# Kernel optimization log

Hardware: AMD Instinct MI355X
Metric: run time of the kernel (lower is better)

## Reference

```python
import jax, jax.numpy as jnp
import numpy as np

N = 20000
E = 320000
IN_DIM, HID, OUT_DIM = 32, 64, 4
HEADS = 4
NEG_SLOPE = 0.2


def _self_loops(src, dst):
    loop = jnp.arange(N, dtype=src.dtype)
    return jnp.concatenate([src, loop]), jnp.concatenate([dst, loop])


def gcn_conv(x, W, b, src, dst):
    h = x @ W                                            # [N, C]
    es, ed = _self_loops(src, dst)
    deg = jax.ops.segment_sum(jnp.ones_like(es, dtype=h.dtype), ed, num_segments=N)
    dinv = jnp.where(deg > 0, jax.lax.rsqrt(deg), 0.0)
    norm = dinv[es] * dinv[ed]                           # [E']
    out = jax.ops.segment_sum(h[es] * norm[:, None], ed, num_segments=N)
    return out + b


def gat_conv(x, W, att_src, att_dst, b, src, dst):
    # PyG GATConv: heads concat, self-loops, leaky_relu(0.2), softmax over incoming edges per dst
    H, C = att_src.shape
    h = (x @ W).reshape(N, H, C)                         # [N, H, C]
    a_s = jnp.sum(h * att_src, axis=-1)                  # [N, H]
    a_d = jnp.sum(h * att_dst, axis=-1)                  # [N, H]
    es, ed = _self_loops(src, dst)
    logits = jax.nn.leaky_relu(a_s[es] + a_d[ed], NEG_SLOPE)   # [E', H]
    m = jax.ops.segment_max(logits, ed, num_segments=N)
    expv = jnp.exp(logits - m[ed])
    denom = jax.ops.segment_sum(expv, ed, num_segments=N)
    alpha = expv / denom[ed]                             # [E', H]
    out = jax.ops.segment_sum(h[es] * alpha[:, :, None], ed, num_segments=N)
    return out.reshape(N, H * C) + b


def setup_inputs() -> dict:
    key = jax.random.key(0)
    ks = iter(jax.random.split(key, 32))
    s = 0.05
    def w(shape):
        return jax.random.normal(next(ks), shape, dtype=jnp.float32) * s
    inp = {}
    inp["x"] = jax.random.normal(next(ks), (N, IN_DIM), dtype=jnp.float32)
    inp["edge_index"] = jax.random.randint(next(ks), (2, E), 0, N, dtype=jnp.int32)
    # encoder1 GCN 32->64; encoder2 GCN 64->128; encoder3 GAT 128->128 x4 heads
    inp["w_e1"], inp["b_e1"] = w((IN_DIM, HID)), jnp.zeros((HID,), jnp.float32)
    inp["w_e2"], inp["b_e2"] = w((HID, 2 * HID)), jnp.zeros((2 * HID,), jnp.float32)
    inp["w_e3"] = w((2 * HID, HEADS * 2 * HID))
    inp["as_e3"], inp["ad_e3"] = w((HEADS, 2 * HID)), w((HEADS, 2 * HID))
    inp["b_e3"] = jnp.zeros((HEADS * 2 * HID,), jnp.float32)
    # decoder1 GCN 1024->128; decoder2 GCN 128->64; decoder3 GAT 64->64 x4 heads
    inp["w_d1"], inp["b_d1"] = w((HEADS * 2 * HID, 2 * HID)), jnp.zeros((2 * HID,), jnp.float32)
    inp["w_d2"], inp["b_d2"] = w((2 * HID, HID)), jnp.zeros((HID,), jnp.float32)
    inp["w_d3"] = w((HID, HEADS * HID))
    inp["as_d3"], inp["ad_d3"] = w((HEADS, HID)), w((HEADS, HID))
    inp["b_d3"] = jnp.zeros((HEADS * HID,), jnp.float32)
    # MLP head 256->256->128->4
    inp["w_fc1"], inp["b_fc1"] = w((4 * HID, 4 * HID)), jnp.zeros((4 * HID,), jnp.float32)
    inp["w_fc2"], inp["b_fc2"] = w((4 * HID, 2 * HID)), jnp.zeros((2 * HID,), jnp.float32)
    inp["w_fin"], inp["b_fin"] = w((2 * HID, OUT_DIM)), jnp.zeros((OUT_DIM,), jnp.float32)
    return inp


def reference(x, edge_index, w_e1, b_e1, w_e2, b_e2, w_e3, as_e3, ad_e3, b_e3,
              w_d1, b_d1, w_d2, b_d2, w_d3, as_d3, ad_d3, b_d3,
              w_fc1, b_fc1, w_fc2, b_fc2, w_fin, b_fin):
    src, dst = edge_index[0], edge_index[1]
    relu = jax.nn.relu
    x1 = relu(gcn_conv(x, w_e1, b_e1, src, dst))
    x2 = relu(gcn_conv(x1, w_e2, b_e2, src, dst))
    x3 = relu(gat_conv(x2, w_e3, as_e3, ad_e3, b_e3, src, dst))
    h = relu(gcn_conv(x3, w_d1, b_d1, src, dst)) + x2
    h = relu(gcn_conv(h, w_d2, b_d2, src, dst)) + x1
    h = relu(gat_conv(h, w_d3, as_d3, ad_d3, b_d3, src, dst))
    h = relu(h @ w_fc1 + b_fc1)
    h = relu(h @ w_fc2 + b_fc2)
    return h @ w_fin + b_fin
```

## Files before the change

### kernel.cpp

```cpp
#include <hip/hip_runtime.h>
#include <cstdint>
#include <cstddef>

static constexpr int Nn = 20000;
static constexpr int Ee = 320000;

typedef _Float16 half8 __attribute__((ext_vector_type(8)));
typedef float f32x4 __attribute__((ext_vector_type(4)));

__device__ __forceinline__ float lrelu02(float x){ return fmaxf(x, 0.2f*x); }

__device__ __forceinline__ void packhl(float v, unsigned short& h, unsigned short& l){
  _Float16 hh = (_Float16)v;
  _Float16 ll = (_Float16)((v - (float)hh) * 2048.0f);
  h = __builtin_bit_cast(unsigned short, hh);
  l = __builtin_bit_cast(unsigned short, ll);
}

__global__ void k_count(const int* __restrict__ dst, int* __restrict__ cnt){
  int e = blockIdx.x*256 + threadIdx.x;
  if (e < Ee) atomicAdd(&cnt[dst[e]], 1);
}

__global__ void k_scan(const int* __restrict__ cnt, int* __restrict__ row_start,
                       float* __restrict__ dinv){
  __shared__ int part[1024];
  int tid = threadIdx.x;
  const int PER = 20;
  int base = tid*PER;
  int s = 0;
  for (int i = 0; i < PER; ++i){ int idx = base+i; if (idx < Nn) s += cnt[idx]; }
  part[tid] = s; __syncthreads();
  for (int off = 1; off < 1024; off <<= 1){
    int v = (tid >= off) ? part[tid-off] : 0;
    __syncthreads();
    part[tid] += v;
    __syncthreads();
  }
  int run = (tid == 0) ? 0 : part[tid-1];
  for (int i = 0; i < PER; ++i){
    int idx = base+i;
    if (idx < Nn){
      row_start[idx] = run;
      int c = cnt[idx];
      run += c;
      dinv[idx] = rsqrtf((float)(c+1));
    }
  }
  if (tid == 1023) row_start[Nn] = run;
}

__global__ void k_scatter(const int* __restrict__ src, const int* __restrict__ dst,
                          const int* __restrict__ row_start, int* __restrict__ fill,
                          int* __restrict__ csr){
  int e = blockIdx.x*256 + threadIdx.x;
  if (e < Ee){
    int d = dst[e];
    int pos = row_start[d] + atomicAdd(&fill[d], 1);
    csr[pos] = src[e];
  }
}

__global__ void k_packw(const float* __restrict__ W, unsigned short* __restrict__ out, int n){
  int i = blockIdx.x*256 + threadIdx.x;
  if (i < n){
    unsigned short h,l; packhl(W[i],h,l);
    out[i] = h; out[i+n] = l;
  }
}

template<int C, int POST>
__global__ __launch_bounds__(256) void k_gcn_agg(
    const float* __restrict__ h, const float* __restrict__ dinv,
    const int* __restrict__ row_start, const int* __restrict__ csr,
    const float* __restrict__ bias, const float* __restrict__ skip,
    float* __restrict__ outf, unsigned short* __restrict__ outp){
  int v = blockIdx.x*4 + (threadIdx.x >> 6);
  int lane = threadIdx.x & 63;
  int s = row_start[v], e = row_start[v+1];
  float dv = dinv[v];
  const int c = (C==32) ? (lane & 31) : ((C==128) ? lane*2 : lane);

  float a0 = 0.f, a1 = 0.f;
  for (int base = s; base < e; base += 64){
    int i = base + lane;
    int u = 0; float du = 0.f;
    if (i < e){ u = csr[i]; du = dinv[u]; }
    int cnt = min(64, e - base);
    int j = 0;
    for (; j + 4 <= cnt; j += 4){
      int u0=__shfl(u,j), u1=__shfl(u,j+1), u2=__shfl(u,j+2), u3=__shfl(u,j+3);
      float d0=__shfl(du,j), d1=__shfl(du,j+1), d2=__shfl(du,j+2), d3=__shfl(du,j+3);
      if constexpr (C == 128){
        float2 t0 = *(const float2*)&h[(size_t)u0*128 + c];
        float2 t1 = *(const float2*)&h[(size_t)u1*128 + c];
        float2 t2 = *(const float2*)&h[(size_t)u2*128 + c];
        float2 t3 = *(const float2*)&h[(size_t)u3*128 + c];
        a0=fmaf(d0,t0.x,a0); a1=fmaf(d0,t0.y,a1);
        a0=fmaf(d1,t1.x,a0); a1=fmaf(d1,t1.y,a1);
        a0=fmaf(d2,t2.x,a0); a1=fmaf(d2,t2.y,a1);
        a0=fmaf(d3,t3.x,a0); a1=fmaf(d3,t3.y,a1);
      } else {
        float t0 = h[(size_t)u0*C + c];
        float t1 = h[(size_t)u1*C + c];
        float t2 = h[(size_t)u2*C + c];
        float t3 = h[(size_t)u3*C + c];
        a0=fmaf(d0,t0,a0); a0=fmaf(d1,t1,a0); a0=fmaf(d2,t2,a0); a0=fmaf(d3,t3,a0);
      }
    }
    for (; j < cnt; ++j){
      int uj = __shfl(u,j); float dj = __shfl(du,j);
      if constexpr (C == 128){
        float2 t = *(const float2*)&h[(size_t)uj*128 + c];
        a0 = fmaf(dj, t.x, a0); a1 = fmaf(dj, t.y, a1);
      } else {
        a0 = fmaf(dj, h[(size_t)uj*C + c], a0);
      }
    }
  }

  if constexpr (C == 128){
    float2 hv = *(const float2*)&h[(size_t)v*128 + c];
    float vx = fmaf(a0, dv, hv.x*dv*dv);
    float vy = fmaf(a1, dv, hv.y*dv*dv);
    if constexpr (POST & 1){
      float2 bv = *(const float2*)&bias[c];
      float2 sk = *(const float2*)&skip[(size_t)v*128 + c];
      vx = fmaxf(vx + bv.x, 0.f) + sk.x;
      vy = fmaxf(vy + bv.y, 0.f) + sk.y;
    }
    if constexpr (POST & 2){
      unsigned short h0,l0,h1,l1; packhl(vx,h0,l0); packhl(vy,h1,l1);
      *(unsigned int*)&outp[(size_t)v*128 + c] = (unsigned)h0 | ((unsigned)h1<<16);
      *(unsigned int*)&outp[(size_t)v*128 + c + (size_t)Nn*128] = (unsigned)l0 | ((unsigned)l1<<16);
    } else {
      *(float2*)&outf[(size_t)v*128 + c] = make_float2(vx, vy);
    }
  } else if constexpr (C == 64){
    float val = fmaf(a0, dv, h[(size_t)v*64 + c]*dv*dv);
    if constexpr (POST & 1){
      val = fmaxf(val + bias[c], 0.f) + skip[(size_t)v*64 + c];
    }
    if constexpr (POST & 2){
      unsigned short hh,ll; packhl(val,hh,ll);
      outp[(size_t)v*64 + c] = hh;
      outp[(size_t)v*64 + c + (size_t)Nn*64] = ll;
    } else {
      outf[(size_t)v*64 + c] = val;
    }
  } else {
    float val = fmaf(a0, dv, h[(size_t)v*32 + c]*dv*dv);
    if (lane < 32){
      unsigned short hh,ll; packhl(val,hh,ll);
      outp[(size_t)v*32 + c] = hh;
      outp[(size_t)v*32 + c + (size_t)Nn*32] = ll;
    }
  }
}

template<int INC, int C>
__global__ void k_fold(const float* __restrict__ W, const float* __restrict__ as_,
                       const float* __restrict__ ad_, float* __restrict__ wsF,
                       float* __restrict__ wdF){
  int h = threadIdx.x >> 6, lane = threadIdx.x & 63;
  for (int k = lane; k < INC; k += 64){
    float s = 0.f, d = 0.f;
    #pragma unroll 4
    for (int c = 0; c < C; ++c){
      float wv = W[(size_t)k*(4*C) + h*C + c];
      s = fmaf(wv, as_[h*C + c], s);
      d = fmaf(wv, ad_[h*C + c], d);
    }
    wsF[h*INC + k] = s;
    wdF[h*INC + k] = d;
  }
}

template<int INC>
__global__ __launch_bounds__(256) void k_attn_in(
    const float* __restrict__ X, const float* __restrict__ wsF, const float* __restrict__ wdF,
    float* __restrict__ aS, float* __restrict__ aD){
  int v = blockIdx.x*4 + (threadIdx.x >> 6);
  int lane = threadIdx.x & 63;
  float x0 = X[(size_t)v*INC + lane];
  float x1 = (INC == 128) ? X[(size_t)v*INC + 64 + lane] : 0.f;
  float s[4], d[4];
  #pragma unroll
  for (int h = 0; h < 4; ++h){
    s[h] = x0*wsF[h*INC + lane];
    d[h] = x0*wdF[h*INC + lane];
    if constexpr (INC == 128){
      s[h] = fmaf(x1, wsF[h*INC + 64 + lane], s[h]);
      d[h] = fmaf(x1, wdF[h*INC + 64 + lane], d[h]);
    }
  }
  #pragma unroll
  for (int off = 32; off; off >>= 1){
    #pragma unroll
    for (int h = 0; h < 4; ++h){
      s[h] += __shfl_xor(s[h], off);
      d[h] += __shfl_xor(d[h], off);
    }
  }
  if (lane == 0){
    *(float4*)&aS[v*4] = make_float4(s[0], s[1], s[2], s[3]);
    *(float4*)&aD[v*4] = make_float4(d[0], d[1], d[2], d[3]);
  }
}

template<int INC>
__global__ __launch_bounds__(256) void k_gat_agg_in(
    const float* __restrict__ X, const float* __restrict__ aS, const float* __restrict__ aD,
    const int* __restrict__ row_start, const int* __restrict__ csr,
    unsigned short* __restrict__ outp){
  int v = blockIdx.x*4 + (threadIdx.x >> 6);
  int lane = threadIdx.x & 63;
  int s0 = row_start[v], e0 = row_start[v+1];

  float4 tD = *(const float4*)&aD[v*4];
  float ad0=tD.x, ad1=tD.y, ad2=tD.z, ad3=tD.w;
  float4 tS = *(const float4*)&aS[v*4];
  float ls0=lrelu02(tS.x+ad0), ls1=lrelu02(tS.y+ad1), ls2=lrelu02(tS.z+ad2), ls3=lrelu02(tS.w+ad3);

  float m0=ls0, m1=ls1, m2=ls2, m3=ls3;
  for (int i = s0 + lane; i < e0; i += 64){
    int u = csr[i];
    float4 a4 = *(const float4*)&aS[u*4];
    m0 = fmaxf(m0, lrelu02(a4.x+ad0));
    m1 = fmaxf(m1, lrelu02(a4.y+ad1));
    m2 = fmaxf(m2, lrelu02(a4.z+ad2));
    m3 = fmaxf(m3, lrelu02(a4.w+ad3));
  }
  #pragma unroll
  for (int off = 32; off; off >>= 1){
    m0 = fmaxf(m0, __shfl_xor(m0, off));
    m1 = fmaxf(m1, __shfl_xor(m1, off));
    m2 = fmaxf(m2, __shfl_xor(m2, off));
    m3 = fmaxf(m3, __shfl_xor(m3, off));
  }

  float sd0=0.f, sd1=0.f, sd2=0.f, sd3=0.f;
  float2 acc0={0,0}, acc1={0,0}, acc2={0,0}, acc3={0,0};
  float ac0=0.f, ac1=0.f, ac2=0.f, ac3=0.f;
  const int c2 = lane*2;

  for (int base = s0; base < e0; base += 64){
    int i = base + lane;
    int u = 0; float e0v=0.f, e1v=0.f, e2v=0.f, e3v=0.f;
    if (i < e0){
      u = csr[i];
      float4 a4 = *(const float4*)&aS[u*4];
      e0v = __expf(lrelu02(a4.x+ad0) - m0);
      e1v = __expf(lrelu02(a4.y+ad1) - m1);
      e2v = __expf(lrelu02(a4.z+ad2) - m2);
      e3v = __expf(lrelu02(a4.w+ad3) - m3);
      sd0 += e0v; sd1 += e1v; sd2 += e2v; sd3 += e3v;
    }
    int cnt = min(64, e0 - base);
    #pragma unroll 2
    for (int j = 0; j < cnt; ++j){
      int uj = __shfl(u, j);
      float f0=__shfl(e0v,j), f1=__shfl(e1v,j), f2=__shfl(e2v,j), f3=__shfl(e3v,j);
      if constexpr (INC == 128){
        float2 xu = *(const float2*)&X[(size_t)uj*128 + c2];
        acc0.x=fmaf(f0,xu.x,acc0.x); acc0.y=fmaf(f0,xu.y,acc0.y);
        acc1.x=fmaf(f1,xu.x,acc1.x); acc1.y=fmaf(f1,xu.y,acc1.y);
        acc2.x=fmaf(f2,xu.x,acc2.x); acc2.y=fmaf(f2,xu.y,acc2.y);
        acc3.x=fmaf(f3,xu.x,acc3.x); acc3.y=fmaf(f3,xu.y,acc3.y);
      } else {
        float xu = X[(size_t)uj*64 + lane];
        ac0=fmaf(f0,xu,ac0); ac1=fmaf(f1,xu,ac1); ac2=fmaf(f2,xu,ac2); ac3=fmaf(f3,xu,ac3);
      }
    }
  }

  #pragma unroll
  for (int off = 32; off; off >>= 1){
    sd0 += __shfl_xor(sd0, off);
    sd1 += __shfl_xor(sd1, off);
    sd2 += __shfl_xor(sd2, off);
    sd3 += __shfl_xor(sd3, off);
  }
  float es0=__expf(ls0-m0), es1=__expf(ls1-m1), es2=__expf(ls2-m2), es3=__expf(ls3-m3);
  float r0=1.f/(sd0+es0), r1=1.f/(sd1+es1), r2=1.f/(sd2+es2), r3=1.f/(sd3+es3);

  if constexpr (INC == 128){
    float2 xv = *(const float2*)&X[(size_t)v*128 + c2];
    const size_t loOff = (size_t)Nn*512;
    float ox, oy; unsigned short h0,l0,h1,l1;
    ox=(acc0.x+es0*xv.x)*r0; oy=(acc0.y+es0*xv.y)*r0;
    packhl(ox,h0,l0); packhl(oy,h1,l1);
    *(unsigned int*)&outp[(size_t)v*512 +   0 + c2] = (unsigned)h0|((unsigned)h1<<16);
    *(unsigned int*)&outp[(size_t)v*512 +   0 + c2 + loOff] = (unsigned)l0|((unsigned)l1<<16);
    ox=(acc1.x+es1*xv.x)*r1; oy=(acc1.y+es1*xv.y)*r1;
    packhl(ox,h0,l0); packhl(oy,h1,l1);
    *(unsigned int*)&outp[(size_t)v*512 + 128 + c2] = (unsigned)h0|((unsigned)h1<<16);
    *(unsigned int*)&outp[(size_t)v*512 + 128 + c2 + loOff] = (unsigned)l0|((unsigned)l1<<16);
    ox=(acc2.x+es2*xv.x)*r2; oy=(acc2.y+es2*xv.y)*r2;
    packhl(ox,h0,l0); packhl(oy,h1,l1);
    *(unsigned int*)&outp[(size_t)v*512 + 256 + c2] = (unsigned)h0|((unsigned)h1<<16);
    *(unsigned int*)&outp[(size_t)v*512 + 256 + c2 + loOff] = (unsigned)l0|((unsigned)l1<<16);
    ox=(acc3.x+es3*xv.x)*r3; oy=(acc3.y+es3*xv.y)*r3;
    packhl(ox,h0,l0); packhl(oy,h1,l1);
    *(unsigned int*)&outp[(size_t)v*512 + 384 + c2] = (unsigned)h0|((unsigned)h1<<16);
    *(unsigned int*)&outp[(size_t)v*512 + 384 + c2 + loOff] = (unsigned)l0|((unsigned)l1<<16);
  } else {
    float xv = X[(size_t)v*64 + lane];
    const size_t loOff = (size_t)Nn*256;
    unsigned short hh,ll;
    float o;
    o = (ac0+es0*xv)*r0; packhl(o,hh,ll);
    outp[(size_t)v*256 +   0 + lane] = hh; outp[(size_t)v*256 +   0 + lane + loOff] = ll;
    o = (ac1+es1*xv)*r1; packhl(o,hh,ll);
    outp[(size_t)v*256 +  64 + lane] = hh; outp[(size_t)v*256 +  64 + lane + loOff] = ll;
    o = (ac2+es2*xv)*r2; packhl(o,hh,ll);
    outp[(size_t)v*256 + 128 + lane] = hh; outp[(size_t)v*256 + 128 + lane + loOff] = ll;
    o = (ac3+es3*xv)*r3; packhl(o,hh,ll);
    outp[(size_t)v*256 + 192 + lane] = hh; outp[(size_t)v*256 + 192 + lane + loOff] = ll;
  }
}

template<int K, int J, int Jh, int EPI>
__global__ __launch_bounds__(256) void k_gemm(
    const unsigned short* __restrict__ Ahi, int lda,
    const unsigned short* __restrict__ Whi,
    const float* __restrict__ bias,
    float* __restrict__ outf, unsigned short* __restrict__ outp){
  __shared__ unsigned short sAhi[2*64*8], sAlo[2*64*8];
  __shared__ unsigned short sBhi[4*64*8], sBlo[4*64*8];

  const int tid  = threadIdx.x;
  const int lane = tid & 63, w = tid >> 6;
  const int rh = w & 1, ch = w >> 1;
  const int rb = blockIdx.x;
  const int colbase = blockIdx.z*Jh + blockIdx.y*64;
  const int akoff   = blockIdx.z*K;
  const size_t AloOff = (size_t)Nn*lda;
  const size_t WloOff = (size_t)K*J;

  f32x4 accH0 = {0,0,0,0}, accH1 = {0,0,0,0};
  f32x4 accM0 = {0,0,0,0}, accM1 = {0,0,0,0};

  const int arow = tid >> 3;
  const int ak4  = (tid & 7) * 4;
  const int aw_idx = (((arow>>4)*4 + (ak4>>3))*16 + (arow&15))*8 + (ak4&4);
  const unsigned short* Ag = Ahi + (size_t)(rb*32 + arow)*lda + akoff + ak4;
  const int bcol = tid & 63;
  const int bkg  = tid >> 6;
  const int bw_idx = (((bcol>>4)*4 + bkg)*16 + (bcol&15))*8;
  const unsigned short* Wg = Whi + colbase + bcol;

  #pragma unroll 1
  for (int ks = 0; ks < K/32; ++ks){
    if (ks) __syncthreads();
    {
      const unsigned short* p = Ag + ks*32;
      uint2 hv = *(const uint2*)p;
      uint2 lv = *(const uint2*)(p + AloOff);
      *(uint2*)&sAhi[aw_idx] = hv;
      *(uint2*)&sAlo[aw_idx] = lv;
    }
    {
      const unsigned short* p = Wg + (size_t)(ks*32 + bkg*8)*J;
      unsigned short h[8], l[8];
      #pragma unroll
      for (int i = 0; i < 8; ++i){
        h[i] = p[(size_t)i*J];
        l[i] = p[(size_t)i*J + WloOff];
      }
      uint4 hv, lv;
      hv.x = (unsigned)h[0]|((unsigned)h[1]<<16); hv.y = (unsigned)h[2]|((unsigned)h[3]<<16);
      hv.z = (unsigned)h[4]|((unsigned)h[5]<<16); hv.w = (unsigned)h[6]|((unsigned)h[7]<<16);
      lv.x = (unsigned)l[0]|((unsigned)l[1]<<16); lv.y = (unsigned)l[2]|((unsigned)l[3]<<16);
      lv.z = (unsigned)l[4]|((unsigned)l[5]<<16); lv.w = (unsigned)l[6]|((unsigned)l[7]<<16);
      *(uint4*)&sBhi[bw_idx] = hv;
      *(uint4*)&sBlo[bw_idx] = lv;
    }
    __syncthreads();

    half8 aH = *(const half8*)&sAhi[(rh*64 + lane)*8];
    half8 aL = *(const half8*)&sAlo[(rh*64 + lane)*8];
    {
      int cf = ch*2;
      half8 bH = *(const half8*)&sBhi[(cf*64 + lane)*8];
      half8 bL = *(const half8*)&sBlo[(cf*64 + lane)*8];
      accH0 = __builtin_amdgcn_mfma_f32_16x16x32_f16(aH, bH, accH0, 0, 0, 0);
      accM0 = __builtin_amdgcn_mfma_f32_16x16x32_f16(aH, bL, accM0, 0, 0, 0);
      accM0 = __builtin_amdgcn_mfma_f32_16x16x32_f16(aL, bH, accM0, 0, 0, 0);
    }
    {
      int cf = ch*2 + 1;
      half8 bH = *(const half8*)&sBhi[(cf*64 + lane)*8];
      half8 bL = *(const half8*)&sBlo[(cf*64 + lane)*8];
      accH1 = __builtin_amdgcn_mfma_f32_16x16x32_f16(aH, bH, accH1, 0, 0, 0);
      accM1 = __builtin_amdgcn_mfma_f32_16x16x32_f16(aH, bL, accM1, 0, 0, 0);
      accM1 = __builtin_amdgcn_mfma_f32_16x16x32_f16(aL, bH, accM1, 0, 0, 0);
    }
  }

  #pragma unroll
  for (int q = 0; q < 2; ++q){
    int cf = ch*2 + q;
    int col = colbase + cf*16 + (lane & 15);
    float bv = (EPI >= 1) ? bias[col] : 0.f;
    const f32x4& aH = q ? accH1 : accH0;
    const f32x4& aM = q ? accM1 : accM0;
    #pragma unroll
    for (int r = 0; r < 4; ++r){
      int row = rb*32 + rh*16 + ((lane>>4)*4 + r);
      float v = aH[r] + aM[r]*(1.0f/2048.0f);
      if constexpr (EPI >= 1) v = fmaxf(v + bv, 0.f);
      if constexpr (EPI == 2){
        unsigned short hh, ll; packhl(v, hh, ll);
        outp[(size_t)row*J + col] = hh;
        outp[(size_t)row*J + col + (size_t)Nn*J] = ll;
      } else {
        outf[(size_t)row*J + col] = v;
      }
    }
  }
}

__global__ __launch_bounds__(256) void k_mm_fin(
    const float* __restrict__ A, const float* __restrict__ W,
    const float* __restrict__ bias, float* __restrict__ out){
  int row = blockIdx.x*4 + (threadIdx.x >> 6);
  int lane = threadIdx.x & 63;
  float a0 = A[(size_t)row*128 + lane];
  float a1 = A[(size_t)row*128 + 64 + lane];
  float4 w0 = ((const float4*)W)[lane];
  float4 w1 = ((const float4*)W)[64 + lane];
  float p0 = fmaf(a1, w1.x, a0*w0.x);
  float p1 = fmaf(a1, w1.y, a0*w0.y);
  float p2 = fmaf(a1, w1.z, a0*w0.z);
  float p3 = fmaf(a1, w1.w, a0*w0.w);
  #pragma unroll
  for (int off = 32; off; off >>= 1){
    p0 += __shfl_xor(p0, off);
    p1 += __shfl_xor(p1, off);
    p2 += __shfl_xor(p2, off);
    p3 += __shfl_xor(p3, off);
  }
  if (lane == 0){
    float4 bv = *(const float4*)bias;
    *(float4*)&out[(size_t)row*4] = make_float4(p0+bv.x, p1+bv.y, p2+bv.z, p3+bv.w);
  }
}

extern "C" void kernel_launch(void* const* d_in, const int* in_sizes, int n_in,
                              void* d_out, int out_size, void* d_ws, size_t ws_size,
                              hipStream_t stream){
  const float* x     = (const float*)d_in[0];
  const int*   ei    = (const int*)  d_in[1];
  const float* w_e1  = (const float*)d_in[2];
  const float* b_e1  = (const float*)d_in[3];
  const float* w_e2  = (const float*)d_in[4];
  const float* b_e2  = (const float*)d_in[5];
  const float* w_e3  = (const float*)d_in[6];
  const float* as_e3 = (const float*)d_in[7];
  const float* ad_e3 = (const float*)d_in[8];
  const float* b_e3  = (const float*)d_in[9];
  const float* w_d1  = (const float*)d_in[10];
  const float* b_d1  = (const float*)d_in[11];
  const float* w_d2  = (const float*)d_in[12];
  const float* b_d2  = (const float*)d_in[13];
  const float* w_d3  = (const float*)d_in[14];
  const float* as_d3 = (const float*)d_in[15];
  const float* ad_d3 = (const float*)d_in[16];
  const float* b_d3  = (const float*)d_in[17];
  const float* w_fc1 = (const float*)d_in[18];
  const float* b_fc1 = (const float*)d_in[19];
  const float* w_fc2 = (const float*)d_in[20];
  const float* b_fc2 = (const float*)d_in[21];
  const float* w_fin = (const float*)d_in[22];
  const float* b_fin = (const float*)d_in[23];

  char* ws = (char*)d_ws;
  size_t off = 0;
  auto alloc = [&](size_t bytes)->char*{
    char* p = ws + off;
    off += (bytes + 127) & ~size_t(127);
    return p;
  };
  int*   cnt       = (int*)  alloc((size_t)Nn*4);
  int*   fill      = (int*)  alloc((size_t)Nn*4);
  int*   row_start = (int*)  alloc((size_t)(Nn+1)*4);
  int*   csr       = (int*)  alloc((size_t)Ee*4);
  float* dinv      = (float*)alloc((size_t)Nn*4);
  float* aSb       = (float*)alloc((size_t)Nn*16);
  float* aDb       = (float*)alloc((size_t)Nn*16);
  float* wsF_e3    = (float*)alloc(4*128*4);
  float* wdF_e3    = (float*)alloc(4*128*4);
  float* wsF_d3    = (float*)alloc(4*64*4);
  float* wdF_d3    = (float*)alloc(4*64*4);
  unsigned short* wp_e1  = (unsigned short*)alloc((size_t)32*64*4);
  unsigned short* wp_e2  = (unsigned short*)alloc((size_t)64*128*4);
  unsigned short* wp_e3  = (unsigned short*)alloc((size_t)128*512*4);
  unsigned short* wp_d1  = (unsigned short*)alloc((size_t)512*128*4);
  unsigned short* wp_d2  = (unsigned short*)alloc((size_t)128*64*4);
  unsigned short* wp_d3  = (unsigned short*)alloc((size_t)64*256*4);
  unsigned short* wp_fc1 = (unsigned short*)alloc((size_t)256*256*4);
  unsigned short* wp_fc2 = (unsigned short*)alloc((size_t)256*128*4);
  unsigned short* P0 = (unsigned short*)alloc((size_t)Nn*32*4);
  float* X1 = (float*)alloc((size_t)Nn*64*4);
  float* X2 = (float*)alloc((size_t)Nn*128*4);
  unsigned short* S1 = (unsigned short*)alloc((size_t)Nn*512*4);
  unsigned short* S2 = (unsigned short*)alloc((size_t)Nn*512*4);
  char*  S3 = alloc((size_t)Nn*128*4);

  const int* srcp = ei;
  const int* dstp = ei + Ee;

  hipMemsetAsync(cnt, 0, (size_t)Nn*4, stream);
  hipMemsetAsync(fill, 0, (size_t)Nn*4, stream);
  k_count<<<(Ee+255)/256, 256, 0, stream>>>(dstp, cnt);
  k_scan<<<1, 1024, 0, stream>>>(cnt, row_start, dinv);
  k_scatter<<<(Ee+255)/256, 256, 0, stream>>>(srcp, dstp, row_start, fill, csr);
  k_fold<128,128><<<1, 256, 0, stream>>>(w_e3, as_e3, ad_e3, wsF_e3, wdF_e3);
  k_fold<64,64><<<1, 256, 0, stream>>>(w_d3, as_d3, ad_d3, wsF_d3, wdF_d3);
  k_packw<<<  8, 256, 0, stream>>>(w_e1,  wp_e1,  32*64);
  k_packw<<< 32, 256, 0, stream>>>(w_e2,  wp_e2,  64*128);
  k_packw<<<256, 256, 0, stream>>>(w_e3,  wp_e3,  128*512);
  k_packw<<<256, 256, 0, stream>>>(w_d1,  wp_d1,  512*128);
  k_packw<<< 32, 256, 0, stream>>>(w_d2,  wp_d2,  128*64);
  k_packw<<< 64, 256, 0, stream>>>(w_d3,  wp_d3,  64*256);
  k_packw<<<256, 256, 0, stream>>>(w_fc1, wp_fc1, 256*256);
  k_packw<<<128, 256, 0, stream>>>(w_fc2, wp_fc2, 256*128);

  k_gcn_agg<32,2><<<Nn/4, 256, 0, stream>>>(x, dinv, row_start, csr, nullptr, nullptr, nullptr, P0);
  k_gemm<32,64,64,1><<<dim3(625,1,1), 256, 0, stream>>>(P0, 32, wp_e1, b_e1, X1, nullptr);
  k_gcn_agg<64,2><<<Nn/4, 256, 0, stream>>>(X1, dinv, row_start, csr, nullptr, nullptr, nullptr, (unsigned short*)S3);
  k_gemm<64,128,128,1><<<dim3(625,2,1), 256, 0, stream>>>((unsigned short*)S3, 64, wp_e2, b_e2, X2, nullptr);
  k_attn_in<128><<<Nn/4, 256, 0, stream>>>(X2, wsF_e3, wdF_e3, aSb, aDb);
  k_gat_agg_in<128><<<Nn/4, 256, 0, stream>>>(X2, aSb, aDb, row_start, csr, S1);
  k_gemm<128,512,128,2><<<dim3(625,2,4), 256, 0, stream>>>(S1, 512, wp_e3, b_e3, nullptr, S2);
  k_gemm<512,128,128,0><<<dim3(625,2,1), 256, 0, stream>>>(S2, 512, wp_d1, nullptr, (float*)S3, nullptr);
  k_gcn_agg<128,3><<<Nn/4, 256, 0, stream>>>((float*)S3, dinv, row_start, csr, b_d1, X2, nullptr, S1);
  k_gemm<128,64,64,0><<<dim3(625,1,1), 256, 0, stream>>>(S1, 128, wp_d2, nullptr, (float*)S2, nullptr);
  k_gcn_agg<64,1><<<Nn/4, 256, 0, stream>>>((float*)S2, dinv, row_start, csr, b_d2, X1, (float*)S3, nullptr);
  k_attn_in<64><<<Nn/4, 256, 0, stream>>>((float*)S3, wsF_d3, wdF_d3, aSb, aDb);
  k_gat_agg_in<64><<<Nn/4, 256, 0, stream>>>((float*)S3, aSb, aDb, row_start, csr, S1);
  k_gemm<64,256,64,2><<<dim3(625,1,4), 256, 0, stream>>>(S1, 256, wp_d3, b_d3, nullptr, S2);
  k_gemm<256,256,256,2><<<dim3(625,4,1), 256, 0, stream>>>(S2, 256, wp_fc1, b_fc1, nullptr, S1);
  k_gemm<256,128,128,1><<<dim3(625,2,1), 256, 0, stream>>>(S1, 256, wp_fc2, b_fc2, (float*)S2, nullptr);
  k_mm_fin<<<Nn/4, 256, 0, stream>>>((float*)S2, w_fin, b_fin, (float*)d_out);
}
```

Baseline: 401.5 us.

## Precompute edge records, split GAT softmax prep, pre-tile GEMM weights

Builds an interleaved (src, dinv[src]) edge record array once, so GCN aggregation reads one record per edge with wave-uniform loads instead of shuffles and a dependent dinv gather. The C=32 case now splits the edges between the two half-waves. GAT aggregation is split into a prep kernel that writes per-edge exp weights and per-node normalisers, followed by a scan-free aggregation kernel. Weights are packed directly into the GEMM's shared-memory tile layout, so B tiles load as 16-byte vectors instead of strided scalar loads. The cost is extra global traffic for the alpha and edge-record arrays and two more kernel launches.

```diff
diff --git a/kernel.cpp b/kernel.cpp
--- a/kernel.cpp
+++ b/kernel.cpp
@@ -9,6 +9,7 @@
 typedef float f32x4 __attribute__((ext_vector_type(4)));
 
 __device__ __forceinline__ float lrelu02(float x){ return fmaxf(x, 0.2f*x); }
+__device__ __forceinline__ float af(int x){ return __int_as_float(x); }
 
 __device__ __forceinline__ void packhl(float v, unsigned short& h, unsigned short& l){
   _Float16 hh = (_Float16)v;
@@ -61,61 +62,88 @@
   }
 }
 
-__global__ void k_packw(const float* __restrict__ W, unsigned short* __restrict__ out, int n){
+__global__ void k_erec(const int* __restrict__ csr, const float* __restrict__ dinv,
+                       int2* __restrict__ erec){
   int i = blockIdx.x*256 + threadIdx.x;
-  if (i < n){
-    unsigned short h,l; packhl(W[i],h,l);
-    out[i] = h; out[i+n] = l;
+  if (i < Ee){
+    int u = csr[i];
+    erec[i] = make_int2(u, __float_as_int(dinv[u]));
+  }
+}
+
+template<int K, int J>
+__global__ void k_packwf(const float* __restrict__ W, unsigned short* __restrict__ out){
+  int i = blockIdx.x*256 + threadIdx.x;
+  if (i < K*J){
+    int k = i / J, col = i - k*J;
+    unsigned short h, l; packhl(W[i], h, l);
+    size_t pos = ((size_t)((col>>4)*(K/8) + (k>>3))*16 + (col&15))*8 + (k&7);
+    out[pos] = h;
+    out[pos + (size_t)K*J] = l;
   }
 }
 
 template<int C, int POST>
 __global__ __launch_bounds__(256) void k_gcn_agg(
     const float* __restrict__ h, const float* __restrict__ dinv,
-    const int* __restrict__ row_start, const int* __restrict__ csr,
+    const int* __restrict__ row_start, const int2* __restrict__ erec,
     const float* __restrict__ bias, const float* __restrict__ skip,
     float* __restrict__ outf, unsigned short* __restrict__ outp){
   int v = blockIdx.x*4 + (threadIdx.x >> 6);
   int lane = threadIdx.x & 63;
-  int s = row_start[v], e = row_start[v+1];
+  int s = __builtin_amdgcn_readfirstlane(row_start[v]);
+  int e = __builtin_amdgcn_readfirstlane(row_start[v+1]);
   float dv = dinv[v];
   const int c = (C==32) ? (lane & 31) : ((C==128) ? lane*2 : lane);
 
   float a0 = 0.f, a1 = 0.f;
-  for (int base = s; base < e; base += 64){
-    int i = base + lane;
-    int u = 0; float du = 0.f;
-    if (i < e){ u = csr[i]; du = dinv[u]; }
-    int cnt = min(64, e - base);
-    int j = 0;
-    for (; j + 4 <= cnt; j += 4){
-      int u0=__shfl(u,j), u1=__shfl(u,j+1), u2=__shfl(u,j+2), u3=__shfl(u,j+3);
-      float d0=__shfl(du,j), d1=__shfl(du,j+1), d2=__shfl(du,j+2), d3=__shfl(du,j+3);
-      if constexpr (C == 128){
-        float2 t0 = *(const float2*)&h[(size_t)u0*128 + c];
-        float2 t1 = *(const float2*)&h[(size_t)u1*128 + c];
-        float2 t2 = *(const float2*)&h[(size_t)u2*128 + c];
-        float2 t3 = *(const float2*)&h[(size_t)u3*128 + c];
-        a0=fmaf(d0,t0.x,a0); a1=fmaf(d0,t0.y,a1);
-        a0=fmaf(d1,t1.x,a0); a1=fmaf(d1,t1.y,a1);
-        a0=fmaf(d2,t2.x,a0); a1=fmaf(d2,t2.y,a1);
-        a0=fmaf(d3,t3.x,a0); a1=fmaf(d3,t3.y,a1);
-      } else {
-        float t0 = h[(size_t)u0*C + c];
-        float t1 = h[(size_t)u1*C + c];
-        float t2 = h[(size_t)u2*C + c];
-        float t3 = h[(size_t)u3*C + c];
-        a0=fmaf(d0,t0,a0); a0=fmaf(d1,t1,a0); a0=fmaf(d2,t2,a0); a0=fmaf(d3,t3,a0);
-      }
-    }
-    for (; j < cnt; ++j){
-      int uj = __shfl(u,j); float dj = __shfl(du,j);
-      if constexpr (C == 128){
-        float2 t = *(const float2*)&h[(size_t)uj*128 + c];
-        a0 = fmaf(dj, t.x, a0); a1 = fmaf(dj, t.y, a1);
-      } else {
-        a0 = fmaf(dj, h[(size_t)uj*C + c], a0);
-      }
+  if constexpr (C == 32){
+    int half = lane >> 5;
+    int j = s + half;
+    for (; j + 2 < e; j += 4){
+      int2 r0 = erec[j], r1 = erec[j+2];
+      float t0 = h[(size_t)r0.x*32 + c];
+      float t1 = h[(size_t)r1.x*32 + c];
+      a0 = fmaf(af(r0.y), t0, a0);
+      a0 = fmaf(af(r1.y), t1, a0);
+    }
+    if (j < e){
+      int2 r0 = erec[j];
+      a0 = fmaf(af(r0.y), h[(size_t)r0.x*32 + c], a0);
+    }
+    a0 += __shfl_xor(a0, 32);
+  } else if constexpr (C == 128){
+    int j = s;
+    for (; j + 4 <= e; j += 4){
+      int2 r0 = erec[j], r1 = erec[j+1], r2 = erec[j+2], r3 = erec[j+3];
+      float2 t0 = *(const float2*)&h[(size_t)r0.x*128 + c];
+      float2 t1 = *(const float2*)&h[(size_t)r1.x*128 + c];
+      float2 t2 = *(const float2*)&h[(size_t)r2.x*128 + c];
+      float2 t3 = *(const float2*)&h[(size_t)r3.x*128 + c];
+      a0=fmaf(af(r0.y),t0.x,a0); a1=fmaf(af(r0.y),t0.y,a1);
+      a0=fmaf(af(r1.y),t1.x,a0); a1=fmaf(af(r1.y),t1.y,a1);
+      a0=fmaf(af(r2.y),t2.x,a0); a1=fmaf(af(r2.y),t2.y,a1);
+      a0=fmaf(af(r3.y),t3.x,a0); a1=fmaf(af(r3.y),t3.y,a1);
+    }
+    for (; j < e; ++j){
+      int2 r = erec[j];
+      float2 t = *(const float2*)&h[(size_t)r.x*128 + c];
+      a0 = fmaf(af(r.y), t.x, a0); a1 = fmaf(af(r.y), t.y, a1);
+    }
+  } else {
+    int j = s;
+    for (; j + 4 <= e; j += 4){
+      int2 r0 = erec[j], r1 = erec[j+1], r2 = erec[j+2], r3 = erec[j+3];
+      float t0 = h[(size_t)r0.x*64 + c];
+      float t1 = h[(size_t)r1.x*64 + c];
+      float t2 = h[(size_t)r2.x*64 + c];
+      float t3 = h[(size_t)r3.x*64 + c];
+      a0=fmaf(af(r0.y),t0,a0); a0=fmaf(af(r1.y),t1,a0);
+      a0=fmaf(af(r2.y),t2,a0); a0=fmaf(af(r3.y),t3,a0);
+    }
+    for (; j < e; ++j){
+      int2 r = erec[j];
+      a0 = fmaf(af(r.y), h[(size_t)r.x*64 + c], a0);
     }
   }
 
@@ -208,14 +236,13 @@
   }
 }
 
-template<int INC>
-__global__ __launch_bounds__(256) void k_gat_agg_in(
-    const float* __restrict__ X, const float* __restrict__ aS, const float* __restrict__ aD,
+__global__ __launch_bounds__(256) void k_gat_prep(
+    const float* __restrict__ aS, const float* __restrict__ aD,
     const int* __restrict__ row_start, const int* __restrict__ csr,
-    unsigned short* __restrict__ outp){
+    float4* __restrict__ alphaE, float4* __restrict__ fS4, float4* __restrict__ rin4){
   int v = blockIdx.x*4 + (threadIdx.x >> 6);
   int lane = threadIdx.x & 63;
-  int s0 = row_start[v], e0 = row_start[v+1];
+  int s = row_start[v], e = row_start[v+1];
 
   float4 tD = *(const float4*)&aD[v*4];
   float ad0=tD.x, ad1=tD.y, ad2=tD.z, ad3=tD.w;
@@ -223,7 +250,7 @@
   float ls0=lrelu02(tS.x+ad0), ls1=lrelu02(tS.y+ad1), ls2=lrelu02(tS.z+ad2), ls3=lrelu02(tS.w+ad3);
 
   float m0=ls0, m1=ls1, m2=ls2, m3=ls3;
-  for (int i = s0 + lane; i < e0; i += 64){
+  for (int i = s + lane; i < e; i += 64){
     int u = csr[i];
     float4 a4 = *(const float4*)&aS[u*4];
     m0 = fmaxf(m0, lrelu02(a4.x+ad0));
@@ -240,40 +267,16 @@
   }
 
   float sd0=0.f, sd1=0.f, sd2=0.f, sd3=0.f;
-  float2 acc0={0,0}, acc1={0,0}, acc2={0,0}, acc3={0,0};
-  float ac0=0.f, ac1=0.f, ac2=0.f, ac3=0.f;
-  const int c2 = lane*2;
-
-  for (int base = s0; base < e0; base += 64){
-    int i = base + lane;
-    int u = 0; float e0v=0.f, e1v=0.f, e2v=0.f, e3v=0.f;
-    if (i < e0){
-      u = csr[i];
-      float4 a4 = *(const float4*)&aS[u*4];
-      e0v = __expf(lrelu02(a4.x+ad0) - m0);
-      e1v = __expf(lrelu02(a4.y+ad1) - m1);
-      e2v = __expf(lrelu02(a4.z+ad2) - m2);
-      e3v = __expf(lrelu02(a4.w+ad3) - m3);
-      sd0 += e0v; sd1 += e1v; sd2 += e2v; sd3 += e3v;
-    }
-    int cnt = min(64, e0 - base);
-    #pragma unroll 2
-    for (int j = 0; j < cnt; ++j){
-      int uj = __shfl(u, j);
-      float f0=__shfl(e0v,j), f1=__shfl(e1v,j), f2=__shfl(e2v,j), f3=__shfl(e3v,j);
-      if constexpr (INC == 128){
-        float2 xu = *(const float2*)&X[(size_t)uj*128 + c2];
-        acc0.x=fmaf(f0,xu.x,acc0.x); acc0.y=fmaf(f0,xu.y,acc0.y);
-        acc1.x=fmaf(f1,xu.x,acc1.x); acc1.y=fmaf(f1,xu.y,acc1.y);
-        acc2.x=fmaf(f2,xu.x,acc2.x); acc2.y=fmaf(f2,xu.y,acc2.y);
-        acc3.x=fmaf(f3,xu.x,acc3.x); acc3.y=fmaf(f3,xu.y,acc3.y);
-      } else {
-        float xu = X[(size_t)uj*64 + lane];
-        ac0=fmaf(f0,xu,ac0); ac1=fmaf(f1,xu,ac1); ac2=fmaf(f2,xu,ac2); ac3=fmaf(f3,xu,ac3);
-      }
-    }
-  }
-
+  for (int i = s + lane; i < e; i += 64){
+    int u = csr[i];
+    float4 a4 = *(const float4*)&aS[u*4];
+    float f0 = __expf(lrelu02(a4.x+ad0) - m0);
+    float f1 = __expf(lrelu02(a4.y+ad1) - m1);
+    float f2 = __expf(lrelu02(a4.z+ad2) - m2);
+    float f3 = __expf(lrelu02(a4.w+ad3) - m3);
+    sd0 += f0; sd1 += f1; sd2 += f2; sd3 += f3;
+    alphaE[i] = make_float4(f0, f1, f2, f3);
+  }
   #pragma unroll
   for (int off = 32; off; off >>= 1){
     sd0 += __shfl_xor(sd0, off);
@@ -281,26 +284,99 @@
     sd2 += __shfl_xor(sd2, off);
     sd3 += __shfl_xor(sd3, off);
   }
-  float es0=__expf(ls0-m0), es1=__expf(ls1-m1), es2=__expf(ls2-m2), es3=__expf(ls3-m3);
-  float r0=1.f/(sd0+es0), r1=1.f/(sd1+es1), r2=1.f/(sd2+es2), r3=1.f/(sd3+es3);
+  if (lane == 0){
+    float es0=__expf(ls0-m0), es1=__expf(ls1-m1), es2=__expf(ls2-m2), es3=__expf(ls3-m3);
+    fS4[v] = make_float4(es0, es1, es2, es3);
+    rin4[v] = make_float4(1.f/(sd0+es0), 1.f/(sd1+es1), 1.f/(sd2+es2), 1.f/(sd3+es3));
+  }
+}
+
+template<int INC>
+__global__ __launch_bounds__(256) void k_gat_agg2(
+    const float* __restrict__ X, const int* __restrict__ csr,
+    const float4* __restrict__ alphaE, const float4* __restrict__ fS4,
+    const float4* __restrict__ rin4, const int* __restrict__ row_start,
+    unsigned short* __restrict__ outp){
+  int v = blockIdx.x*4 + (threadIdx.x >> 6);
+  int lane = threadIdx.x & 63;
+  int s = __builtin_amdgcn_readfirstlane(row_start[v]);
+  int e = __builtin_amdgcn_readfirstlane(row_start[v+1]);
+  const int c2 = lane*2;
+
+  float2 acc0={0,0}, acc1={0,0}, acc2={0,0}, acc3={0,0};
+  float ac0=0.f, ac1=0.f, ac2=0.f, ac3=0.f;
+
+  int j = s;
+  for (; j + 4 <= e; j += 4){
+    int u0=csr[j], u1=csr[j+1], u2=csr[j+2], u3=csr[j+3];
+    float4 f0=alphaE[j], f1=alphaE[j+1], f2=alphaE[j+2], f3=alphaE[j+3];
+    if constexpr (INC == 128){
+      float2 x0 = *(const float2*)&X[(size_t)u0*128 + c2];
+      float2 x1 = *(const float2*)&X[(size_t)u1*128 + c2];
+      float2 x2 = *(const float2*)&X[(size_t)u2*128 + c2];
+      float2 x3 = *(const float2*)&X[(size_t)u3*128 + c2];
+      acc0.x=fmaf(f0.x,x0.x,acc0.x); acc0.y=fmaf(f0.x,x0.y,acc0.y);
+      acc1.x=fmaf(f0.y,x0.x,acc1.x); acc1.y=fmaf(f0.y,x0.y,acc1.y);
+      acc2.x=fmaf(f0.z,x0.x,acc2.x); acc2.y=fmaf(f0.z,x0.y,acc2.y);
+      acc3.x=fmaf(f0.w,x0.x,acc3.x); acc3.y=fmaf(f0.w,x0.y,acc3.y);
+      acc0.x=fmaf(f1.x,x1.x,acc0.x); acc0.y=fmaf(f1.x,x1.y,acc0.y);
+      acc1.x=fmaf(f1.y,x1.x,acc1.x); acc1.y=fmaf(f1.y,x1.y,acc1.y);
+      acc2.x=fmaf(f1.z,x1.x,acc2.x); acc2.y=fmaf(f1.z,x1.y,acc2.y);
+      acc3.x=fmaf(f1.w,x1.x,acc3.x); acc3.y=fmaf(f1.w,x1.y,acc3.y);
+      acc0.x=fmaf(f2.x,x2.x,acc0.x); acc0.y=fmaf(f2.x,x2.y,acc0.y);
+      acc1.x=fmaf(f2.y,x2.x,acc1.x); acc1.y=fmaf(f2.y,x2.y,acc1.y);
+      acc2.x=fmaf(f2.z,x2.x,acc2.x); acc2.y=fmaf(f2.z,x2.y,acc2.y);
+      acc3.x=fmaf(f2.w,x2.x,acc3.x); acc3.y=fmaf(f2.w,x2.y,acc3.y);
+      acc0.x=fmaf(f3.x,x3.x,acc0.x); acc0.y=fmaf(f3.x,x3.y,acc0.y);
+      acc1.x=fmaf(f3.y,x3.x,acc1.x); acc1.y=fmaf(f3.y,x3.y,acc1.y);
+      acc2.x=fmaf(f3.z,x3.x,acc2.x); acc2.y=fmaf(f3.z,x3.y,acc2.y);
+      acc3.x=fmaf(f3.w,x3.x,acc3.x); acc3.y=fmaf(f3.w,x3.y,acc3.y);
+    } else {
+      float x0 = X[(size_t)u0*64 + lane];
+      float x1 = X[(size_t)u1*64 + lane];
+      float x2 = X[(size_t)u2*64 + lane];
+      float x3 = X[(size_t)u3*64 + lane];
+      ac0=fmaf(f0.x,x0,ac0); ac1=fmaf(f0.y,x0,ac1); ac2=fmaf(f0.z,x0,ac2); ac3=fmaf(f0.w,x0,ac3);
+      ac0=fmaf(f1.x,x1,ac0); ac1=fmaf(f1.y,x1,ac1); ac2=fmaf(f1.z,x1,ac2); ac3=fmaf(f1.w,x1,ac3);
+      ac0=fmaf(f2.x,x2,ac0); ac1=fmaf(f2.y,x2,ac1); ac2=fmaf(f2.z,x2,ac2); ac3=fmaf(f2.w,x2,ac3);
+      ac0=fmaf(f3.x,x3,ac0); ac1=fmaf(f3.y,x3,ac1); ac2=fmaf(f3.z,x3,ac2); ac3=fmaf(f3.w,x3,ac3);
+    }
+  }
+  for (; j < e; ++j){
+    int u = csr[j];
+    float4 f = alphaE[j];
+    if constexpr (INC == 128){
+      float2 xu = *(const float2*)&X[(size_t)u*128 + c2];
+      acc0.x=fmaf(f.x,xu.x,acc0.x); acc0.y=fmaf(f.x,xu.y,acc0.y);
+      acc1.x=fmaf(f.y,xu.x,acc1.x); acc1.y=fmaf(f.y,xu.y,acc1.y);
+      acc2.x=fmaf(f.z,xu.x,acc2.x); acc2.y=fmaf(f.z,xu.y,acc2.y);
+      acc3.x=fmaf(f.w,xu.x,acc3.x); acc3.y=fmaf(f.w,xu.y,acc3.y);
+    } else {
+      float xu = X[(size_t)u*64 + lane];
+      ac0=fmaf(f.x,xu,ac0); ac1=fmaf(f.y,xu,ac1); ac2=fmaf(f.z,xu,ac2); ac3=fmaf(f.w,xu,ac3);
+    }
+  }
+
+  float4 fs = fS4[v];
+  float4 rv = rin4[v];
 
   if constexpr (INC == 128){
     float2 xv = *(const float2*)&X[(size_t)v*128 + c2];
     const size_t loOff = (size_t)Nn*512;
     float ox, oy; unsigned short h0,l0,h1,l1;
-    ox=(acc0.x+es0*xv.x)*r0; oy=(acc0.y+es0*xv.y)*r0;
+    ox=(acc0.x+fs.x*xv.x)*rv.x; oy=(acc0.y+fs.x*xv.y)*rv.x;
     packhl(ox,h0,l0); packhl(oy,h1,l1);
     *(unsigned int*)&outp[(size_t)v*512 +   0 + c2] = (unsigned)h0|((unsigned)h1<<16);
     *(unsigned int*)&outp[(size_t)v*512 +   0 + c2 + loOff] = (unsigned)l0|((unsigned)l1<<16);
-    ox=(acc1.x+es1*xv.x)*r1; oy=(acc1.y+es1*xv.y)*r1;
+    ox=(acc1.x+fs.y*xv.x)*rv.y; oy=(acc1.y+fs.y*xv.y)*rv.y;
     packhl(ox,h0,l0); packhl(oy,h1,l1);
     *(unsigned int*)&outp[(size_t)v*512 + 128 + c2] = (unsigned)h0|((unsigned)h1<<16);
     *(unsigned int*)&outp[(size_t)v*512 + 128 + c2 + loOff] = (unsigned)l0|((unsigned)l1<<16);
-    ox=(acc2.x+es2*xv.x)*r2; oy=(acc2.y+es2*xv.y)*r2;
+    ox=(acc2.x+fs.z*xv.x)*rv.z; oy=(acc2.y+fs.z*xv.y)*rv.z;
     packhl(ox,h0,l0); packhl(oy,h1,l1);
     *(unsigned int*)&outp[(size_t)v*512 + 256 + c2] = (unsigned)h0|((unsigned)h1<<16);
     *(unsigned int*)&outp[(size_t)v*512 + 256 + c2 + loOff] = (unsigned)l0|((unsigned)l1<<16);
-    ox=(acc3.x+es3*xv.x)*r3; oy=(acc3.y+es3*xv.y)*r3;
+    ox=(acc3.x+fs.w*xv.x)*rv.w; oy=(acc3.y+fs.w*xv.y)*rv.w;
     packhl(ox,h0,l0); packhl(oy,h1,l1);
     *(unsigned int*)&outp[(size_t)v*512 + 384 + c2] = (unsigned)h0|((unsigned)h1<<16);
     *(unsigned int*)&outp[(size_t)v*512 + 384 + c2 + loOff] = (unsigned)l0|((unsigned)l1<<16);
@@ -309,13 +385,13 @@
     const size_t loOff = (size_t)Nn*256;
     unsigned short hh,ll;
     float o;
-    o = (ac0+es0*xv)*r0; packhl(o,hh,ll);
+    o = (ac0+fs.x*xv)*rv.x; packhl(o,hh,ll);
     outp[(size_t)v*256 +   0 + lane] = hh; outp[(size_t)v*256 +   0 + lane + loOff] = ll;
-    o = (ac1+es1*xv)*r1; packhl(o,hh,ll);
+    o = (ac1+fs.y*xv)*rv.y; packhl(o,hh,ll);
     outp[(size_t)v*256 +  64 + lane] = hh; outp[(size_t)v*256 +  64 + lane + loOff] = ll;
-    o = (ac2+es2*xv)*r2; packhl(o,hh,ll);
+    o = (ac2+fs.z*xv)*rv.z; packhl(o,hh,ll);
     outp[(size_t)v*256 + 128 + lane] = hh; outp[(size_t)v*256 + 128 + lane + loOff] = ll;
-    o = (ac3+es3*xv)*r3; packhl(o,hh,ll);
+    o = (ac3+fs.w*xv)*rv.w; packhl(o,hh,ll);
     outp[(size_t)v*256 + 192 + lane] = hh; outp[(size_t)v*256 + 192 + lane + loOff] = ll;
   }
 }
@@ -323,7 +399,7 @@
 template<int K, int J, int Jh, int EPI>
 __global__ __launch_bounds__(256) void k_gemm(
     const unsigned short* __restrict__ Ahi, int lda,
-    const unsigned short* __restrict__ Whi,
+    const unsigned short* __restrict__ Wp,
     const float* __restrict__ bias,
     float* __restrict__ outf, unsigned short* __restrict__ outp){
   __shared__ unsigned short sAhi[2*64*8], sAlo[2*64*8];
@@ -348,7 +424,8 @@
   const int bcol = tid & 63;
   const int bkg  = tid >> 6;
   const int bw_idx = (((bcol>>4)*4 + bkg)*16 + (bcol&15))*8;
-  const unsigned short* Wg = Whi + colbase + bcol;
+  const int cf_g  = (colbase>>4) + (bcol>>4);
+  const size_t wbase = ((size_t)cf_g*(K/8)*16 + (size_t)(bcol&15))*8;
 
   #pragma unroll 1
   for (int ks = 0; ks < K/32; ++ks){
@@ -361,18 +438,9 @@
       *(uint2*)&sAlo[aw_idx] = lv;
     }
     {
-      const unsigned short* p = Wg + (size_t)(ks*32 + bkg*8)*J;
-      unsigned short h[8], l[8];
-      #pragma unroll
-      for (int i = 0; i < 8; ++i){
-        h[i] = p[(size_t)i*J];
-        l[i] = p[(size_t)i*J + WloOff];
-      }
-      uint4 hv, lv;
-      hv.x = (unsigned)h[0]|((unsigned)h[1]<<16); hv.y = (unsigned)h[2]|((unsigned)h[3]<<16);
-      hv.z = (unsigned)h[4]|((unsigned)h[5]<<16); hv.w = (unsigned)h[6]|((unsigned)h[7]<<16);
-      lv.x = (unsigned)l[0]|((unsigned)l[1]<<16); lv.y = (unsigned)l[2]|((unsigned)l[3]<<16);
-      lv.z = (unsigned)l[4]|((unsigned)l[5]<<16); lv.w = (unsigned)l[6]|((unsigned)l[7]<<16);
+      size_t goff = wbase + (size_t)(ks*4 + bkg)*16*8;
+      uint4 hv = *(const uint4*)&Wp[goff];
+      uint4 lv = *(const uint4*)&Wp[goff + WloOff];
       *(uint4*)&sBhi[bw_idx] = hv;
       *(uint4*)&sBlo[bw_idx] = lv;
     }
@@ -487,6 +555,10 @@
   int*   row_start = (int*)  alloc((size_t)(Nn+1)*4);
   int*   csr       = (int*)  alloc((size_t)Ee*4);
   float* dinv      = (float*)alloc((size_t)Nn*4);
+  int2*  erec      = (int2*) alloc((size_t)Ee*8);
+  float4* alphaE   = (float4*)alloc((size_t)Ee*16);
+  float4* fS4      = (float4*)alloc((size_t)Nn*16);
+  float4* rin4     = (float4*)alloc((size_t)Nn*16);
   float* aSb       = (float*)alloc((size_t)Nn*16);
   float* aDb       = (float*)alloc((size_t)Nn*16);
   float* wsF_e3    = (float*)alloc(4*128*4);
@@ -516,30 +588,33 @@
   k_count<<<(Ee+255)/256, 256, 0, stream>>>(dstp, cnt);
   k_scan<<<1, 1024, 0, stream>>>(cnt, row_start, dinv);
   k_scatter<<<(Ee+255)/256, 256, 0, stream>>>(srcp, dstp, row_start, fill, csr);
+  k_erec<<<(Ee+255)/256, 256, 0, stream>>>(csr, dinv, erec);
   k_fold<128,128><<<1, 256, 0, stream>>>(w_e3, as_e3, ad_e3, wsF_e3, wdF_e3);
   k_fold<64,64><<<1, 256, 0, stream>>>(w_d3, as_d3, ad_d3, wsF_d3, wdF_d3);
-  k_packw<<<  8, 256, 0, stream>>>(w_e1,  wp_e1,  32*64);
-  k_packw<<< 32, 256, 0, stream>>>(w_e2,  wp_e2,  64*128);
-  k_packw<<<256, 256, 0, stream>>>(w_e3,  wp_e3,  128*512);
-  k_packw<<<256, 256, 0, stream>>>(w_d1,  wp_d1,  512*128);
-  k_packw<<< 32, 256, 0, stream>>>(w_d2,  wp_d2,  128*64);
-  k_packw<<< 64, 256, 0, stream>>>(w_d3,  wp_d3,  64*256);
-  k_packw<<<256, 256, 0, stream>>>(w_fc1, wp_fc1, 256*256);
-  k_packw<<<128, 256, 0, stream>>>(w_fc2, wp_fc2, 256*128);
-
-  k_gcn_agg<32,2><<<Nn/4, 256, 0, stream>>>(x, dinv, row_start, csr, nullptr, nullptr, nullptr, P0);
+  k_packwf<32,64>  <<<  8, 256, 0, stream>>>(w_e1,  wp_e1);
+  k_packwf<64,128> <<< 32, 256, 0, stream>>>(w_e2,  wp_e2);
+  k_packwf<128,512><<<256, 256, 0, stream>>>(w_e3,  wp_e3);
+  k_packwf<512,128><<<256, 256, 0, stream>>>(w_d1,  wp_d1);
+  k_packwf<128,64> <<< 32, 256, 0, stream>>>(w_d2,  wp_d2);
+  k_packwf<64,256> <<< 64, 256, 0, stream>>>(w_d3,  wp_d3);
+  k_packwf<256,256><<<256, 256, 0, stream>>>(w_fc1, wp_fc1);
+  k_packwf<256,128><<<128, 256, 0, stream>>>(w_fc2, wp_fc2);
+
+  k_gcn_agg<32,2><<<Nn/4, 256, 0, stream>>>(x, dinv, row_start, erec, nullptr, nullptr, nullptr, P0);
   k_gemm<32,64,64,1><<<dim3(625,1,1), 256, 0, stream>>>(P0, 32, wp_e1, b_e1, X1, nullptr);
-  k_gcn_agg<64,2><<<Nn/4, 256, 0, stream>>>(X1, dinv, row_start, csr, nullptr, nullptr, nullptr, (unsigned short*)S3);
+  k_gcn_agg<64,2><<<Nn/4, 256, 0, stream>>>(X1, dinv, row_start, erec, nullptr, nullptr, nullptr, (unsigned short*)S3);
   k_gemm<64,128,128,1><<<dim3(625,2,1), 256, 0, stream>>>((unsigned short*)S3, 64, wp_e2, b_e2, X2, nullptr);
   k_attn_in<128><<<Nn/4, 256, 0, stream>>>(X2, wsF_e3, wdF_e3, aSb, aDb);
-  k_gat_agg_in<128><<<Nn/4, 256, 0, stream>>>(X2, aSb, aDb, row_start, csr, S1);
+  k_gat_prep<<<Nn/4, 256, 0, stream>>>(aSb, aDb, row_start, csr, alphaE, fS4, rin4);
+  k_gat_agg2<128><<<Nn/4, 256, 0, stream>>>(X2, csr, alphaE, fS4, rin4, row_start, S1);
   k_gemm<128,512,128,2><<<dim3(625,2,4), 256, 0, stream>>>(S1, 512, wp_e3, b_e3, nullptr, S2);
   k_gemm<512,128,128,0><<<dim3(625,2,1), 256, 0, stream>>>(S2, 512, wp_d1, nullptr, (float*)S3, nullptr);
-  k_gcn_agg<128,3><<<Nn/4, 256, 0, stream>>>((float*)S3, dinv, row_start, csr, b_d1, X2, nullptr, S1);
+  k_gcn_agg<128,3><<<Nn/4, 256, 0, stream>>>((float*)S3, dinv, row_start, erec, b_d1, X2, nullptr, S1);
   k_gemm<128,64,64,0><<<dim3(625,1,1), 256, 0, stream>>>(S1, 128, wp_d2, nullptr, (float*)S2, nullptr);
-  k_gcn_agg<64,1><<<Nn/4, 256, 0, stream>>>((float*)S2, dinv, row_start, csr, b_d2, X1, (float*)S3, nullptr);
+  k_gcn_agg<64,1><<<Nn/4, 256, 0, stream>>>((float*)S2, dinv, row_start, erec, b_d2, X1, (float*)S3, nullptr);
   k_attn_in<64><<<Nn/4, 256, 0, stream>>>((float*)S3, wsF_d3, wdF_d3, aSb, aDb);
-  k_gat_agg_in<64><<<Nn/4, 256, 0, stream>>>((float*)S3, aSb, aDb, row_start, csr, S1);
+  k_gat_prep<<<Nn/4, 256, 0, stream>>>(aSb, aDb, row_start, csr, alphaE, fS4, rin4);
+  k_gat_agg2<64><<<Nn/4, 256, 0, stream>>>((float*)S3, csr, alphaE, fS4, rin4, row_start, S1);
   k_gemm<64,256,64,2><<<dim3(625,1,4), 256, 0, stream>>>(S1, 256, wp_d3, b_d3, nullptr, S2);
   k_gemm<256,256,256,2><<<dim3(625,4,1), 256, 0, stream>>>(S2, 256, wp_fc1, b_fc1, nullptr, S1);
   k_gemm<256,128,128,1><<<dim3(625,2,1), 256, 0, stream>>>(S1, 256, wp_fc2, b_fc2, (float*)S2, nullptr);
```

After: 396.2 us. Within noise of the previous version (-1.3%).
